# Performance work log

Hardware: AMD Instinct MI355X
Metric: run time of the kernel (lower is better)

## Reference

```python
import jax, jax.numpy as jnp
import numpy as np

POS_DIM = 60  # position_embed_dim


def sincos_pos_embed(pos, dim):
    # pos: [..., 3] -> [..., dim]; dim//3 channels per coordinate, half sin / half cos
    d = dim // 3            # 20
    half = d // 2           # 10
    omega = 1.0 / (10000.0 ** (jnp.arange(half, dtype=pos.dtype) / half))
    out = pos[..., None] * omega                     # [..., 3, half]
    emb = jnp.concatenate([jnp.sin(out), jnp.cos(out)], axis=-1)  # [..., 3, d]
    return emb.reshape(pos.shape[:-1] + (3 * d,))


def setup_inputs() -> dict:
    key = jax.random.key(0)
    ks = jax.random.split(key, 20)
    B, N, K = 2, 16384, 24
    d_points, d_model = 64, 128
    s = 0.02
    inp = {
        "features": jax.random.normal(ks[0], (B, N, d_points), jnp.float32),
        "xyz": jax.random.normal(ks[1], (B, N, 3), jnp.float32),
        "knn_idx": jax.random.randint(ks[2], (B, N, K), 0, N),
        "knn_xyz": jax.random.normal(ks[3], (B, N, K, 3), jnp.float32),
        "fc1_w": jax.random.normal(ks[4], (d_points, d_model), jnp.float32) * s,
        "fc1_b": jnp.zeros((d_model,), jnp.float32),
        "fc2_w": jax.random.normal(ks[5], (d_model, d_model), jnp.float32) * s,
        "fc2_b": jnp.zeros((d_model,), jnp.float32),
        "d1_w": jax.random.normal(ks[6], (POS_DIM, d_model), jnp.float32) * s,
        "d1_b": jnp.zeros((d_model,), jnp.float32),
        "d2_w": jax.random.normal(ks[7], (d_model, d_model), jnp.float32) * s,
        "d2_b": jnp.zeros((d_model,), jnp.float32),
        "g1_w": jax.random.normal(ks[8], (d_model, d_model), jnp.float32) * s,
        "g1_b": jnp.zeros((d_model,), jnp.float32),
        "g2_w": jax.random.normal(ks[9], (d_model, d_model), jnp.float32) * s,
        "g2_b": jnp.zeros((d_model,), jnp.float32),
    }
    return inp


def reference(features, xyz, knn_idx, knn_xyz,
              fc1_w, fc1_b, fc2_w, fc2_b,
              d1_w, d1_b, d2_w, d2_b,
              g1_w, g1_b, g2_w, g2_b):
    B = features.shape[0]
    x = features @ fc1_w + fc1_b                       # [B,N,D]
    # index_points: gather neighbor features (q=x, k=v=gathered)
    kv = x[jnp.arange(B)[:, None, None], knn_idx]      # [B,N,K,D]
    g_xyz = xyz[:, :, None] - knn_xyz                  # [B,N,K,3]
    g_emb = sincos_pos_embed(g_xyz, POS_DIM)           # [B,N,K,60]
    pos_enc = jax.nn.relu(g_emb @ d1_w + d1_b) @ d2_w + d2_b   # [B,N,K,D]
    h = x[:, :, None] - kv + pos_enc                   # [B,N,K,D]
    attn = jax.nn.relu(h @ g1_w + g1_b) @ g2_w + g2_b  # [B,N,K,D]
    attn = jax.nn.softmax(attn / np.sqrt(kv.shape[-1]), axis=-2)  # softmax over K
    res = jnp.einsum('bmnf,bmnf->bmf', attn, kv + pos_enc)
    res = res @ fc2_w + fc2_b + x
    return res, attn
```

## Files before the change

### kernel.cpp

```cpp
#include <hip/hip_runtime.h>
#include <hip/hip_bf16.h>
#include <math.h>

constexpr int BB = 2;
constexpr int NN = 16384;
constexpr int KK = 24;
constexpr int DM = 128;
constexpr int DP = 64;

constexpr int PPB = 4;
constexpr int RR  = PPB * KK;

typedef __bf16 v8bf __attribute__((ext_vector_type(8)));
typedef float  v4f  __attribute__((ext_vector_type(4)));

constexpr int LDA128 = 136;
constexpr int LDA64  = 72;

constexpr int OFF_FC1T = 0;
constexpr int OFF_D1T  = 8192;
constexpr int OFF_D2T  = 16384;
constexpr int OFF_G1T  = 32768;
constexpr int OFF_G2T  = 49152;
constexpr int OFF_FC2T = 65536;
constexpr int W_TOTAL  = 81920;

__global__ __launch_bounds__(256) void prep_kernel(
    const float* __restrict__ fc1_w, const float* __restrict__ fc2_w,
    const float* __restrict__ d1_w,  const float* __restrict__ d2_w,
    const float* __restrict__ g1_w,  const float* __restrict__ g2_w,
    __hip_bfloat16* __restrict__ wbuf)
{
    const int i = blockIdx.x * 256 + threadIdx.x;
    if (i >= W_TOTAL) return;
    float v;
    if (i < OFF_D1T) {
        const int j = i, n = j >> 6, k = j & 63;
        v = fc1_w[k * DM + n];
    } else if (i < OFF_D2T) {
        const int j = i - OFF_D1T, n = j >> 6, k = j & 63;
        v = (k < 60) ? d1_w[k * DM + n] : 0.f;
    } else if (i < OFF_G1T) {
        const int j = i - OFF_D2T, n = j >> 7, k = j & 127;
        v = d2_w[k * DM + n];
    } else if (i < OFF_G2T) {
        const int j = i - OFF_G1T, n = j >> 7, k = j & 127;
        v = g1_w[k * DM + n];
    } else if (i < OFF_FC2T) {
        const int j = i - OFF_G2T, n = j >> 7, k = j & 127;
        v = g2_w[k * DM + n];
    } else {
        const int j = i - OFF_FC2T, f = j >> 7, g = j & 127;
        v = fc2_w[g * DM + f];
    }
    wbuf[i] = __float2bfloat16(v);
}

template <int MT, int NKT, int LDA, int LDB>
__device__ __forceinline__ void mm_frags(
    const __hip_bfloat16* As, const __hip_bfloat16* __restrict__ Bt,
    int c0, int lane, v4f (&acc)[MT][2])
{
    const int ln = lane & 15, quad = lane >> 4;
    #pragma unroll
    for (int mt = 0; mt < MT; ++mt) {
        acc[mt][0] = (v4f)0.f;
        acc[mt][1] = (v4f)0.f;
    }
    __builtin_amdgcn_s_setprio(1);
    #pragma unroll
    for (int kt = 0; kt < NKT; ++kt) {
        const int k0 = kt * 32 + quad * 8;
        const v8bf b0 = *(const v8bf*)(Bt + (c0 + ln) * LDB + k0);
        const v8bf b1 = *(const v8bf*)(Bt + (c0 + 16 + ln) * LDB + k0);
        #pragma unroll
        for (int mt = 0; mt < MT; ++mt) {
            const v8bf a = *(const v8bf*)(As + (mt * 16 + ln) * LDA + k0);
            acc[mt][0] = __builtin_amdgcn_mfma_f32_16x16x32_bf16(a, b0, acc[mt][0], 0, 0, 0);
            acc[mt][1] = __builtin_amdgcn_mfma_f32_16x16x32_bf16(a, b1, acc[mt][1], 0, 0, 0);
        }
    }
    __builtin_amdgcn_s_setprio(0);
}

__global__ __launch_bounds__(256) void fc1_kernel(
    const float* __restrict__ feat,
    const __hip_bfloat16* __restrict__ fc1t,
    const float* __restrict__ fc1_b,
    __hip_bfloat16* __restrict__ x_bf)
{
    __shared__ alignas(16) __hip_bfloat16 s_f[32 * LDA64];
    const int tid = threadIdx.x;
    const int r0  = blockIdx.x * 32;
    for (int e = tid; e < 32 * DP; e += 256) {
        const int r = e >> 6, k = e & 63;
        s_f[r * LDA64 + k] = __float2bfloat16(feat[(size_t)(r0 + r) * DP + k]);
    }
    __syncthreads();
    const int w = tid >> 6, lane = tid & 63;
    const int ln = lane & 15, quad = lane >> 4;
    const int c0 = w * 32;
    v4f acc[2][2];
    mm_frags<2, 2, LDA64, 64>(s_f, fc1t, c0, lane, acc);
    #pragma unroll
    for (int nl = 0; nl < 2; ++nl) {
        const int col = c0 + nl * 16 + ln;
        const float bb = fc1_b[col];
        #pragma unroll
        for (int mt = 0; mt < 2; ++mt)
            #pragma unroll
            for (int r = 0; r < 4; ++r) {
                const int row = mt * 16 + quad * 4 + r;
                x_bf[(size_t)(r0 + row) * DM + col] = __float2bfloat16(acc[mt][nl][r] + bb);
            }
    }
}

__device__ __forceinline__ int zoff(int row, int col) {
    return (row << 7) + ((((col >> 3) ^ row) & 15) << 3) + (col & 7);
}

__global__ __launch_bounds__(256, 3) void fused_kernel(
    const __hip_bfloat16* __restrict__ x_bf,
    const float* __restrict__ xyz,
    const int*   __restrict__ knn_idx,
    const float* __restrict__ knn_xyz,
    const __hip_bfloat16* __restrict__ wbuf,
    const float* __restrict__ d1_b, const float* __restrict__ d2_b,
    const float* __restrict__ g1_b, const float* __restrict__ g2_b,
    const float* __restrict__ fc2_b,
    float* __restrict__ out_res,
    float* __restrict__ out_attn)
{
    __shared__ alignas(16) __hip_bfloat16 s_A[RR * LDA128];
    __shared__ alignas(16) __hip_bfloat16 s_Z[RR * DM];
    __shared__ alignas(16) __hip_bfloat16 s_xm[PPB * DM];

    __hip_bfloat16* s_ge = s_A;
    int* s_idx = reinterpret_cast<int*>(s_A + RR * LDA64);

    const int tid = threadIdx.x;
    const int pt0 = blockIdx.x * PPB;
    const int b   = pt0 >> 14;
    const int w = tid >> 6, lane = tid & 63;
    const int ln = lane & 15, quad = lane >> 4;
    const int c0 = w * 32;

    if (tid < RR) s_idx[tid] = knn_idx[(size_t)pt0 * KK + tid];
    if (tid < PPB * DM / 8)
        *reinterpret_cast<v8bf*>(s_xm + tid * 8) =
            *(const v8bf*)(x_bf + (size_t)pt0 * DM + tid * 8);
    if (tid < RR)
        *reinterpret_cast<uint2*>(s_ge + tid * LDA64 + 60) = make_uint2(0u, 0u);
    for (int e = tid; e < RR * 30; e += 256) {
        const int row = e / 30;
        const int rem = e - row * 30;
        const int c = rem / 10;
        const int i = rem - c * 10;
        const int g = pt0 + row / 24;
        const float pv = xyz[(size_t)g * 3 + c] - knn_xyz[((size_t)pt0 * KK + row) * 3 + c];
        const float om = exp2f(-(float)i * 1.3287712379549449f);
        float sv, cv;
        __sincosf(pv * om, &sv, &cv);
        s_ge[row * LDA64 + c * 20 + i]      = __float2bfloat16(sv);
        s_ge[row * LDA64 + c * 20 + 10 + i] = __float2bfloat16(cv);
    }
    __syncthreads();

    v4f acc[6][2];

    v8bf gv[6];
    {
        const size_t xbase = (size_t)b * NN * DM;
        #pragma unroll
        for (int i = 0; i < 6; ++i) {
            const int e = tid + i * 256;
            const int row = e >> 4, part = e & 15;
            gv[i] = *(const v8bf*)(x_bf + xbase + (size_t)s_idx[row] * DM + part * 8);
        }
    }
    mm_frags<6, 2, LDA64, 64>(s_A, wbuf + OFF_D1T, c0, lane, acc);
    #pragma unroll
    for (int i = 0; i < 6; ++i) {
        const int e = tid + i * 256;
        const int row = e >> 4, part = e & 15;
        *reinterpret_cast<v8bf*>(&s_Z[zoff(row, part * 8)]) = gv[i];
    }
    __syncthreads();
    {
        const float bb0 = d1_b[c0 + ln], bb1 = d1_b[c0 + 16 + ln];
        #pragma unroll
        for (int mt = 0; mt < 6; ++mt) {
            const int row0 = mt * 16 + quad * 4;
            #pragma unroll
            for (int r = 0; r < 4; ++r) {
                s_A[(row0 + r) * LDA128 + c0 + ln]      = __float2bfloat16(fmaxf(acc[mt][0][r] + bb0, 0.f));
                s_A[(row0 + r) * LDA128 + c0 + 16 + ln] = __float2bfloat16(fmaxf(acc[mt][1][r] + bb1, 0.f));
            }
        }
    }
    __syncthreads();

    mm_frags<6, 4, LDA128, DM>(s_A, wbuf + OFF_D2T, c0, lane, acc);
    __syncthreads();
    {
        const float bb0 = d2_b[c0 + ln], bb1 = d2_b[c0 + 16 + ln];
        #pragma unroll
        for (int mt = 0; mt < 6; ++mt) {
            const int row0 = mt * 16 + quad * 4;
            const int p = row0 / 24;
            const float xm0 = __bfloat162float(s_xm[p * DM + c0 + ln]);
            const float xm1 = __bfloat162float(s_xm[p * DM + c0 + 16 + ln]);
            #pragma unroll
            for (int r = 0; r < 4; ++r) {
                const int row = row0 + r;
                const int zo0 = zoff(row, c0 + ln);
                const int zo1 = zoff(row, c0 + 16 + ln);
                const float pe0 = acc[mt][0][r] + bb0;
                const float pe1 = acc[mt][1][r] + bb1;
                const float kv0 = __bfloat162float(s_Z[zo0]);
                const float kv1 = __bfloat162float(s_Z[zo1]);
                s_A[row * LDA128 + c0 + ln]      = __float2bfloat16(xm0 - kv0 + pe0);
                s_A[row * LDA128 + c0 + 16 + ln] = __float2bfloat16(xm1 - kv1 + pe1);
                s_Z[zo0] = __float2bfloat16(kv0 + pe0);
                s_Z[zo1] = __float2bfloat16(kv1 + pe1);
            }
        }
    }
    __syncthreads();

    mm_frags<6, 4, LDA128, DM>(s_A, wbuf + OFF_G1T, c0, lane, acc);
    __syncthreads();
    {
        const float bb0 = g1_b[c0 + ln], bb1 = g1_b[c0 + 16 + ln];
        #pragma unroll
        for (int mt = 0; mt < 6; ++mt) {
            const int row0 = mt * 16 + quad * 4;
            #pragma unroll
            for (int r = 0; r < 4; ++r) {
                s_A[(row0 + r) * LDA128 + c0 + ln]      = __float2bfloat16(fmaxf(acc[mt][0][r] + bb0, 0.f));
                s_A[(row0 + r) * LDA128 + c0 + 16 + ln] = __float2bfloat16(fmaxf(acc[mt][1][r] + bb1, 0.f));
            }
        }
    }
    __syncthreads();

    mm_frags<6, 4, LDA128, DM>(s_A, wbuf + OFF_G2T, c0, lane, acc);
    __syncthreads();
    {
        const float iscl = 0.08838834764831845f;
        const float bb0 = g2_b[c0 + ln], bb1 = g2_b[c0 + 16 + ln];
        #pragma unroll
        for (int mt = 0; mt < 6; ++mt) {
            const int row0 = mt * 16 + quad * 4;
            #pragma unroll
            for (int r = 0; r < 4; ++r) {
                s_A[(row0 + r) * LDA128 + c0 + ln]      = __float2bfloat16((acc[mt][0][r] + bb0) * iscl);
                s_A[(row0 + r) * LDA128 + c0 + 16 + ln] = __float2bfloat16((acc[mt][1][r] + bb1) * iscl);
            }
        }
    }
    __syncthreads();

    float rres[2];
    #pragma unroll
    for (int cc = 0; cc < 2; ++cc) {
        const int ch = cc * 256 + tid;
        const int p = ch >> 7, f = ch & 127;
        const int rbase = p * KK;
        float lv[KK];
        float mx = -1e30f;
        #pragma unroll
        for (int n = 0; n < KK; ++n) {
            lv[n] = __bfloat162float(s_A[(rbase + n) * LDA128 + f]);
            mx = fmaxf(mx, lv[n]);
        }
        float sum = 0.f;
        #pragma unroll
        for (int n = 0; n < KK; ++n) {
            const float ev = __expf(lv[n] - mx);
            lv[n] = ev;
            sum += ev;
        }
        const float inv = 1.f / sum;
        float racc = 0.f;
        float* ab = out_attn + (size_t)(pt0 + p) * KK * DM + f;
        #pragma unroll
        for (int n = 0; n < KK; ++n) {
            const float a = lv[n] * inv;
            ab[n * DM] = a;
            racc = fmaf(a, __bfloat162float(s_Z[zoff(rbase + n, f)]), racc);
        }
        rres[cc] = racc;
    }
    __syncthreads();
    #pragma unroll
    for (int cc = 0; cc < 2; ++cc) {
        const int ch = cc * 256 + tid;
        const int p = ch >> 7, f = ch & 127;
        s_A[p * LDA128 + f] = __float2bfloat16(rres[cc]);
    }
    __syncthreads();

    {
        v4f a2[1][2];
        mm_frags<1, 4, LDA128, DM>(s_A, wbuf + OFF_FC2T, c0, lane, a2);
        if (quad == 0) {
            #pragma unroll
            for (int nl = 0; nl < 2; ++nl) {
                const int col = c0 + nl * 16 + ln;
                const float bb = fc2_b[col];
                #pragma unroll
                for (int r = 0; r < 4; ++r)
                    out_res[(size_t)(pt0 + r) * DM + col] =
                        a2[0][nl][r] + bb + __bfloat162float(s_xm[r * DM + col]);
            }
        }
    }
}

extern "C" void kernel_launch(void* const* d_in, const int* in_sizes, int n_in,
                              void* d_out, int out_size, void* d_ws, size_t ws_size,
                              hipStream_t stream)
{
    const float* features = (const float*)d_in[0];
    const float* xyz      = (const float*)d_in[1];
    const int*   knn_idx  = (const int*)  d_in[2];
    const float* knn_xyz  = (const float*)d_in[3];
    const float* fc1_w    = (const float*)d_in[4];
    const float* fc1_b    = (const float*)d_in[5];
    const float* fc2_w    = (const float*)d_in[6];
    const float* fc2_b    = (const float*)d_in[7];
    const float* d1_w     = (const float*)d_in[8];
    const float* d1_b     = (const float*)d_in[9];
    const float* d2_w     = (const float*)d_in[10];
    const float* d2_b     = (const float*)d_in[11];
    const float* g1_w     = (const float*)d_in[12];
    const float* g1_b     = (const float*)d_in[13];
    const float* g2_w     = (const float*)d_in[14];
    const float* g2_b     = (const float*)d_in[15];

    __hip_bfloat16* x_bf = (__hip_bfloat16*)d_ws;
    __hip_bfloat16* wbuf = x_bf + (size_t)BB * NN * DM;
    float* out_res  = (float*)d_out;
    float* out_attn = out_res + (size_t)BB * NN * DM;

    prep_kernel<<<(W_TOTAL + 255) / 256, 256, 0, stream>>>(
        fc1_w, fc2_w, d1_w, d2_w, g1_w, g2_w, wbuf);
    fc1_kernel<<<(BB * NN) / 32, 256, 0, stream>>>(
        features, wbuf + OFF_FC1T, fc1_b, x_bf);
    fused_kernel<<<(BB * NN) / PPB, 256, 0, stream>>>(
        x_bf, xyz, knn_idx, knn_xyz, wbuf,
        d1_b, d2_b, g1_b, g2_b, fc2_b, out_res, out_attn);
}
```

Measured before the change: 675.9 us.

## Fuse softmax and weighted sum into MFMA accumulator registers

Runs the softmax over K and the attention-weighted sum of kv+pos_enc directly on the g2 matmul accumulators. Max and sum reductions across the 16-row tiles use lane shuffles, and the kv+pe values are kept packed as bf16 in registers instead of being written back to shared memory. This removes a shared-memory round trip of logits, a barrier, and the per-thread column softmax pass. It also changes the zoff swizzle. Register pressure rises from the packed kv array, and the attn store pattern changes to 4 rows per lane per 16-column group.

```diff
diff --git a/kernel.cpp b/kernel.cpp
--- a/kernel.cpp
+++ b/kernel.cpp
@@ -117,7 +117,21 @@
 }
 
 __device__ __forceinline__ int zoff(int row, int col) {
-    return (row << 7) + ((((col >> 3) ^ row) & 15) << 3) + (col & 7);
+    const int h = (row + (row >> 3)) & 15;
+    return (row << 7) + ((((col >> 3) ^ h) & 15) << 3) + (col & 7);
+}
+
+__device__ __forceinline__ unsigned pk2(float a, float b) {
+    __hip_bfloat16 ha = __float2bfloat16(a), hb = __float2bfloat16(b);
+    unsigned ua = *reinterpret_cast<unsigned short*>(&ha);
+    unsigned ub = *reinterpret_cast<unsigned short*>(&hb);
+    return ua | (ub << 16);
+}
+__device__ __forceinline__ float unlo(unsigned u) {
+    unsigned v = u << 16; return *reinterpret_cast<float*>(&v);
+}
+__device__ __forceinline__ float unhi(unsigned u) {
+    unsigned v = u & 0xffff0000u; return *reinterpret_cast<float*>(&v);
 }
 
 __global__ __launch_bounds__(256, 3) void fused_kernel(
@@ -145,6 +159,7 @@
     const int w = tid >> 6, lane = tid & 63;
     const int ln = lane & 15, quad = lane >> 4;
     const int c0 = w * 32;
+    const bool lo = (quad < 2);
 
     if (tid < RR) s_idx[tid] = knn_idx[(size_t)pt0 * KK + tid];
     if (tid < PPB * DM / 8)
@@ -203,28 +218,34 @@
 
     mm_frags<6, 4, LDA128, DM>(s_A, wbuf + OFF_D2T, c0, lane, acc);
     __syncthreads();
+    unsigned kvpk[6][2][2];
     {
         const float bb0 = d2_b[c0 + ln], bb1 = d2_b[c0 + 16 + ln];
         #pragma unroll
         for (int mt = 0; mt < 6; ++mt) {
+            constexpr int pl_[6] = {0,0,1,2,2,3};
+            constexpr int ph_[6] = {0,1,1,2,3,3};
             const int row0 = mt * 16 + quad * 4;
-            const int p = row0 / 24;
+            const int p = (pl_[mt] == ph_[mt]) ? pl_[mt] : (lo ? pl_[mt] : ph_[mt]);
             const float xm0 = __bfloat162float(s_xm[p * DM + c0 + ln]);
             const float xm1 = __bfloat162float(s_xm[p * DM + c0 + 16 + ln]);
+            float kp0[4], kp1[4];
             #pragma unroll
             for (int r = 0; r < 4; ++r) {
                 const int row = row0 + r;
-                const int zo0 = zoff(row, c0 + ln);
-                const int zo1 = zoff(row, c0 + 16 + ln);
                 const float pe0 = acc[mt][0][r] + bb0;
                 const float pe1 = acc[mt][1][r] + bb1;
-                const float kv0 = __bfloat162float(s_Z[zo0]);
-                const float kv1 = __bfloat162float(s_Z[zo1]);
+                const float kv0 = __bfloat162float(s_Z[zoff(row, c0 + ln)]);
+                const float kv1 = __bfloat162float(s_Z[zoff(row, c0 + 16 + ln)]);
                 s_A[row * LDA128 + c0 + ln]      = __float2bfloat16(xm0 - kv0 + pe0);
                 s_A[row * LDA128 + c0 + 16 + ln] = __float2bfloat16(xm1 - kv1 + pe1);
-                s_Z[zo0] = __float2bfloat16(kv0 + pe0);
-                s_Z[zo1] = __float2bfloat16(kv1 + pe1);
-            }
+                kp0[r] = kv0 + pe0;
+                kp1[r] = kv1 + pe1;
+            }
+            kvpk[mt][0][0] = pk2(kp0[0], kp0[1]);
+            kvpk[mt][0][1] = pk2(kp0[2], kp0[3]);
+            kvpk[mt][1][0] = pk2(kp1[0], kp1[1]);
+            kvpk[mt][1][1] = pk2(kp1[2], kp1[3]);
         }
     }
     __syncthreads();
@@ -246,59 +267,130 @@
     __syncthreads();
 
     mm_frags<6, 4, LDA128, DM>(s_A, wbuf + OFF_G2T, c0, lane, acc);
-    __syncthreads();
-    {
-        const float iscl = 0.08838834764831845f;
-        const float bb0 = g2_b[c0 + ln], bb1 = g2_b[c0 + 16 + ln];
+    {
+        const float C = 0.08838834764831845f * 1.4426950408889634f;
+        const float sb0 = g2_b[c0 + ln] * C, sb1 = g2_b[c0 + 16 + ln] * C;
+        #pragma unroll
+        for (int mt = 0; mt < 6; ++mt)
+            #pragma unroll
+            for (int r = 0; r < 4; ++r) {
+                acc[mt][0][r] = fmaf(acc[mt][0][r], C, sb0);
+                acc[mt][1][r] = fmaf(acc[mt][1][r], C, sb1);
+            }
+
+        constexpr int pl_[6] = {0,0,1,2,2,3};
+        constexpr int ph_[6] = {0,1,1,2,3,3};
+
+        float mx[4][2];
+        #pragma unroll
+        for (int p = 0; p < 4; ++p) { mx[p][0] = -1e30f; mx[p][1] = -1e30f; }
+        #pragma unroll
+        for (int mt = 0; mt < 6; ++mt)
+            #pragma unroll
+            for (int nl = 0; nl < 2; ++nl) {
+                const float m4 = fmaxf(fmaxf(acc[mt][nl][0], acc[mt][nl][1]),
+                                       fmaxf(acc[mt][nl][2], acc[mt][nl][3]));
+                if (pl_[mt] == ph_[mt]) {
+                    mx[pl_[mt]][nl] = fmaxf(mx[pl_[mt]][nl], m4);
+                } else {
+                    mx[pl_[mt]][nl] = fmaxf(mx[pl_[mt]][nl], lo ? m4 : -1e30f);
+                    mx[ph_[mt]][nl] = fmaxf(mx[ph_[mt]][nl], lo ? -1e30f : m4);
+                }
+            }
+        #pragma unroll
+        for (int p = 0; p < 4; ++p)
+            #pragma unroll
+            for (int nl = 0; nl < 2; ++nl) {
+                float v = mx[p][nl];
+                v = fmaxf(v, __shfl_xor(v, 16));
+                v = fmaxf(v, __shfl_xor(v, 32));
+                mx[p][nl] = v;
+            }
+
+        float sm[4][2];
+        #pragma unroll
+        for (int p = 0; p < 4; ++p) { sm[p][0] = 0.f; sm[p][1] = 0.f; }
+        #pragma unroll
+        for (int mt = 0; mt < 6; ++mt)
+            #pragma unroll
+            for (int nl = 0; nl < 2; ++nl) {
+                const float mxv = (pl_[mt] == ph_[mt]) ? mx[pl_[mt]][nl]
+                                  : (lo ? mx[pl_[mt]][nl] : mx[ph_[mt]][nl]);
+                float es = 0.f;
+                #pragma unroll
+                for (int r = 0; r < 4; ++r) {
+                    const float e = exp2f(acc[mt][nl][r] - mxv);
+                    acc[mt][nl][r] = e;
+                    es += e;
+                }
+                if (pl_[mt] == ph_[mt]) {
+                    sm[pl_[mt]][nl] += es;
+                } else {
+                    sm[pl_[mt]][nl] += lo ? es : 0.f;
+                    sm[ph_[mt]][nl] += lo ? 0.f : es;
+                }
+            }
+        #pragma unroll
+        for (int p = 0; p < 4; ++p)
+            #pragma unroll
+            for (int nl = 0; nl < 2; ++nl) {
+                float v = sm[p][nl];
+                v += __shfl_xor(v, 16);
+                v += __shfl_xor(v, 32);
+                sm[p][nl] = 1.f / v;
+            }
+
+        float rp[4][2];
+        #pragma unroll
+        for (int p = 0; p < 4; ++p) { rp[p][0] = 0.f; rp[p][1] = 0.f; }
+        float* abase = out_attn + (size_t)pt0 * KK * DM;
         #pragma unroll
         for (int mt = 0; mt < 6; ++mt) {
-            const int row0 = mt * 16 + quad * 4;
-            #pragma unroll
-            for (int r = 0; r < 4; ++r) {
-                s_A[(row0 + r) * LDA128 + c0 + ln]      = __float2bfloat16((acc[mt][0][r] + bb0) * iscl);
-                s_A[(row0 + r) * LDA128 + c0 + 16 + ln] = __float2bfloat16((acc[mt][1][r] + bb1) * iscl);
-            }
-        }
-    }
-    __syncthreads();
-
-    float rres[2];
-    #pragma unroll
-    for (int cc = 0; cc < 2; ++cc) {
-        const int ch = cc * 256 + tid;
-        const int p = ch >> 7, f = ch & 127;
-        const int rbase = p * KK;
-        float lv[KK];
-        float mx = -1e30f;
-        #pragma unroll
-        for (int n = 0; n < KK; ++n) {
-            lv[n] = __bfloat162float(s_A[(rbase + n) * LDA128 + f]);
-            mx = fmaxf(mx, lv[n]);
-        }
-        float sum = 0.f;
-        #pragma unroll
-        for (int n = 0; n < KK; ++n) {
-            const float ev = __expf(lv[n] - mx);
-            lv[n] = ev;
-            sum += ev;
-        }
-        const float inv = 1.f / sum;
-        float racc = 0.f;
-        float* ab = out_attn + (size_t)(pt0 + p) * KK * DM + f;
-        #pragma unroll
-        for (int n = 0; n < KK; ++n) {
-            const float a = lv[n] * inv;
-            ab[n * DM] = a;
-            racc = fmaf(a, __bfloat162float(s_Z[zoff(rbase + n, f)]), racc);
-        }
-        rres[cc] = racc;
-    }
-    __syncthreads();
-    #pragma unroll
-    for (int cc = 0; cc < 2; ++cc) {
-        const int ch = cc * 256 + tid;
-        const int p = ch >> 7, f = ch & 127;
-        s_A[p * LDA128 + f] = __float2bfloat16(rres[cc]);
+            const int rowg0 = mt * 16 + quad * 4;
+            #pragma unroll
+            for (int nl = 0; nl < 2; ++nl) {
+                const int col = c0 + nl * 16 + ln;
+                const float invv = (pl_[mt] == ph_[mt]) ? sm[pl_[mt]][nl]
+                                   : (lo ? sm[pl_[mt]][nl] : sm[ph_[mt]][nl]);
+                const float kv0 = unlo(kvpk[mt][nl][0]);
+                const float kv1 = unhi(kvpk[mt][nl][0]);
+                const float kv2 = unlo(kvpk[mt][nl][1]);
+                const float kv3 = unhi(kvpk[mt][nl][1]);
+                const float a0 = acc[mt][nl][0] * invv;
+                const float a1 = acc[mt][nl][1] * invv;
+                const float a2 = acc[mt][nl][2] * invv;
+                const float a3 = acc[mt][nl][3] * invv;
+                abase[(size_t)(rowg0 + 0) * DM + col] = a0;
+                abase[(size_t)(rowg0 + 1) * DM + col] = a1;
+                abase[(size_t)(rowg0 + 2) * DM + col] = a2;
+                abase[(size_t)(rowg0 + 3) * DM + col] = a3;
+                const float ws = fmaf(a0, kv0, fmaf(a1, kv1, fmaf(a2, kv2, a3 * kv3)));
+                if (pl_[mt] == ph_[mt]) {
+                    rp[pl_[mt]][nl] += ws;
+                } else {
+                    rp[pl_[mt]][nl] += lo ? ws : 0.f;
+                    rp[ph_[mt]][nl] += lo ? 0.f : ws;
+                }
+            }
+        }
+        #pragma unroll
+        for (int p = 0; p < 4; ++p)
+            #pragma unroll
+            for (int nl = 0; nl < 2; ++nl) {
+                float v = rp[p][nl];
+                v += __shfl_xor(v, 16);
+                v += __shfl_xor(v, 32);
+                rp[p][nl] = v;
+            }
+
+        __syncthreads();
+        if (quad == 0) {
+            #pragma unroll
+            for (int p = 0; p < 4; ++p) {
+                s_A[p * LDA128 + c0 + ln]      = __float2bfloat16(rp[p][0]);
+                s_A[p * LDA128 + c0 + 16 + ln] = __float2bfloat16(rp[p][1]);
+            }
+        }
     }
     __syncthreads();
 
```

New measurement: 670.5 us. About the same (-0.8%).
